# Optimization experiments

Measured on AMD Instinct MI355X. Metric: run time of the kernel, lower is better.

Reference implementation:

```python
import jax, jax.numpy as jnp
import numpy as np

C = 16            # cell state dim
ALPHA_T = 0.1     # alive threshold
_SOBEL = jnp.array([[-1., 0., 1.], [-2., 0., 2.], [-1., 0., 1.]], jnp.float32) / 8.0


def _depthwise(x, k2d):
    # x: [B,H,W,C], k2d: [3,3] same filter per channel (groups=C depthwise conv)
    k = jnp.tile(k2d[:, :, None, None], (1, 1, 1, C)).astype(x.dtype)  # [3,3,1,C] HWIO
    return jax.lax.conv_general_dilated(
        x, k, window_strides=(1, 1), padding='SAME',
        feature_group_count=C, dimension_numbers=('NHWC', 'HWIO', 'NHWC'))


def _alive_mask(state):
    # 3x3 max-pool on alpha channel (index 3), stride 1, SAME padding
    alpha = state[..., 3:4]
    pooled = jax.lax.reduce_window(alpha, -jnp.inf, jax.lax.max,
                                   (1, 3, 3, 1), (1, 1, 1, 1), 'SAME')
    return (pooled >= ALPHA_T).astype(state.dtype)


def setup_inputs() -> dict:
    key = jax.random.key(0)
    k1, k2, k3, k4, k5 = jax.random.split(key, 5)
    B, H, W, S = 128, 40, 40, 32
    initial_state = jax.random.uniform(k1, (B, H, W, C), jnp.float32)
    # MLP params (torch Linear layout: [out, in]); scaled to keep 32-step rollout finite
    W1 = jax.random.normal(k2, (128, 3 * C), jnp.float32) * 0.1
    b1 = jax.random.normal(k3, (128,), jnp.float32) * 0.1
    W2 = jax.random.normal(k4, (C, 128), jnp.float32) * 0.02
    # Bernoulli(0.5) stochastic update mask == (rand > update_probability=0.5)
    upd_mask = jax.random.randint(k5, (S, B, H, W), 0, 2, jnp.int32)
    return {"initial_state": initial_state, "W1": W1, "b1": b1, "W2": W2,
            "upd_mask": upd_mask, "steps": S, "batch_size": B}


def reference(initial_state, W1, b1, W2, upd_mask, steps, batch_size):
    def step(state, mask_t):
        am = _alive_mask(state)
        masked = state * am
        sx = _depthwise(masked, _SOBEL)
        sy = _depthwise(masked, _SOBEL.T)
        perception = jnp.concatenate([masked, sx, sy], axis=-1)       # [B,H,W,48]
        hid = jax.nn.relu(jnp.einsum('bhwi,oi->bhwo', perception, W1) + b1)
        update = jnp.einsum('bhwi,oi->bhwo', hid, W2)                 # [B,H,W,16]
        update = update * mask_t[..., None].astype(state.dtype)
        new_state = state + update
        new_state = new_state * _alive_mask(new_state)
        return new_state, new_state

    _, ys = jax.lax.scan(step, initial_state, upd_mask)
    stacked = jnp.concatenate([initial_state[None], ys], axis=0)      # [steps+1,B,H,W,16]
    alpha = jnp.clip(stacked[..., 3:4], 0.0, 1.0)
    rgb = (jnp.clip(1.0 - alpha + stacked[..., :3], 0.0, 1.0) * 255.0).astype(jnp.uint8)
    return rgb, stacked
```

## Files before the change

kernel.cpp:

```cpp
#include <hip/hip_runtime.h>

#define Cn 16
#define Bn 128
#define Hn 40
#define Wn 40
#define Sn 32
#define HID 128
#define PIX (Bn * Hn * Wn)
#define NFRAME (Sn + 1)
#define RGB_TOTAL (NFRAME * PIX * 3)
#define STACK_FRAME (PIX * Cn)
#define ALPHA_T 0.1f

__global__ __launch_bounds__(256) void step_update(
    const float* __restrict__ S,
    const float* __restrict__ amF,
    const int*   __restrict__ maskT,
    float*       __restrict__ P,
    float*       __restrict__ Pa,
    const float* __restrict__ W1,
    const float* __restrict__ b1,
    const float* __restrict__ W2T)
{
    int idx = blockIdx.x * 256 + threadIdx.x;
    int x  = idx % Wn;
    int t1 = idx / Wn;
    int y  = t1 % Hn;

    float am[3][3];
#pragma unroll
    for (int dy = 0; dy < 3; ++dy) {
#pragma unroll
        for (int dx = 0; dx < 3; ++dx) {
            int yy = y + dy - 1, xx = x + dx - 1;
            bool in = (yy >= 0) && (yy < Hn) && (xx >= 0) && (xx < Wn);
            am[dy][dx] = in ? amF[idx + (dy - 1) * Wn + (dx - 1)] : 0.f;
        }
    }

    float perc[48];
    float4 cen[4];
#pragma unroll
    for (int cg = 0; cg < 4; ++cg) {
        float4 m[3][3];
#pragma unroll
        for (int dy = 0; dy < 3; ++dy) {
#pragma unroll
            for (int dx = 0; dx < 3; ++dx) {
                int yy = y + dy - 1, xx = x + dx - 1;
                bool in = (yy >= 0) && (yy < Hn) && (xx >= 0) && (xx < Wn);
                float4 v;
                if (in) {
                    v = *(const float4*)&S[(idx + (dy - 1) * Wn + (dx - 1)) * Cn + cg * 4];
                    if (dy == 1 && dx == 1) cen[cg] = v;
                    float a = am[dy][dx];
                    v.x *= a; v.y *= a; v.z *= a; v.w *= a;
                } else {
                    v.x = 0.f; v.y = 0.f; v.z = 0.f; v.w = 0.f;
                }
                m[dy][dx] = v;
            }
        }
        perc[cg * 4 + 0] = m[1][1].x;
        perc[cg * 4 + 1] = m[1][1].y;
        perc[cg * 4 + 2] = m[1][1].z;
        perc[cg * 4 + 3] = m[1][1].w;
        perc[16 + cg * 4 + 0] = ((m[0][2].x - m[0][0].x) + 2.f * (m[1][2].x - m[1][0].x) + (m[2][2].x - m[2][0].x)) * 0.125f;
        perc[16 + cg * 4 + 1] = ((m[0][2].y - m[0][0].y) + 2.f * (m[1][2].y - m[1][0].y) + (m[2][2].y - m[2][0].y)) * 0.125f;
        perc[16 + cg * 4 + 2] = ((m[0][2].z - m[0][0].z) + 2.f * (m[1][2].z - m[1][0].z) + (m[2][2].z - m[2][0].z)) * 0.125f;
        perc[16 + cg * 4 + 3] = ((m[0][2].w - m[0][0].w) + 2.f * (m[1][2].w - m[1][0].w) + (m[2][2].w - m[2][0].w)) * 0.125f;
        perc[32 + cg * 4 + 0] = ((m[2][0].x - m[0][0].x) + 2.f * (m[2][1].x - m[0][1].x) + (m[2][2].x - m[0][2].x)) * 0.125f;
        perc[32 + cg * 4 + 1] = ((m[2][0].y - m[0][0].y) + 2.f * (m[2][1].y - m[0][1].y) + (m[2][2].y - m[0][2].y)) * 0.125f;
        perc[32 + cg * 4 + 2] = ((m[2][0].z - m[0][0].z) + 2.f * (m[2][1].z - m[0][1].z) + (m[2][2].z - m[0][2].z)) * 0.125f;
        perc[32 + cg * 4 + 3] = ((m[2][0].w - m[0][0].w) + 2.f * (m[2][1].w - m[0][1].w) + (m[2][2].w - m[0][2].w)) * 0.125f;
    }

    float upd[16];
#pragma unroll
    for (int c = 0; c < 16; ++c) upd[c] = 0.f;

    for (int j = 0; j < HID; ++j) {
        const float* w = &W1[j * 48];
        float hh0 = b1[j], hh1 = 0.f, hh2 = 0.f, hh3 = 0.f;
#pragma unroll
        for (int i = 0; i < 12; ++i) {
            hh0 = fmaf(perc[i],      w[i],      hh0);
            hh1 = fmaf(perc[12 + i], w[12 + i], hh1);
            hh2 = fmaf(perc[24 + i], w[24 + i], hh2);
            hh3 = fmaf(perc[36 + i], w[36 + i], hh3);
        }
        float h = fmaxf((hh0 + hh1) + (hh2 + hh3), 0.f);

        const float* w2 = &W2T[j * 16];
#pragma unroll
        for (int c = 0; c < 16; ++c) upd[c] = fmaf(h, w2[c], upd[c]);
    }

    float fm = (float)maskT[idx];

#pragma unroll
    for (int cg = 0; cg < 4; ++cg) {
        float4 s = cen[cg];
        float4 o;
        o.x = s.x + upd[cg * 4 + 0] * fm;
        o.y = s.y + upd[cg * 4 + 1] * fm;
        o.z = s.z + upd[cg * 4 + 2] * fm;
        o.w = s.w + upd[cg * 4 + 3] * fm;
        *(float4*)&P[idx * Cn + cg * 4] = o;
        if (cg == 0) Pa[idx] = o.w;
    }
}

__global__ __launch_bounds__(256) void step_mask(
    const float* __restrict__ P,
    const float* __restrict__ Pa,
    float*       __restrict__ Snext,
    float*       __restrict__ amNext)
{
    int idx = blockIdx.x * 256 + threadIdx.x;
    int x  = idx % Wn;
    int t1 = idx / Wn;
    int y  = t1 % Hn;

    float a[5][5];
#pragma unroll
    for (int dy = 0; dy < 5; ++dy) {
#pragma unroll
        for (int dx = 0; dx < 5; ++dx) {
            int yy = y + dy - 2, xx = x + dx - 2;
            bool in = (yy >= 0) && (yy < Hn) && (xx >= 0) && (xx < Wn);
            a[dy][dx] = in ? Pa[idx + (dy - 2) * Wn + (dx - 2)] : -1e30f;
        }
    }

    float s[3][3];
    float aliveC = 0.f;
#pragma unroll
    for (int qy = 0; qy < 3; ++qy) {
#pragma unroll
        for (int qx = 0; qx < 3; ++qx) {
            float p = a[qy][qx];
            p = fmaxf(p, a[qy][qx + 1]);
            p = fmaxf(p, a[qy][qx + 2]);
            p = fmaxf(p, a[qy + 1][qx]);
            p = fmaxf(p, a[qy + 1][qx + 1]);
            p = fmaxf(p, a[qy + 1][qx + 2]);
            p = fmaxf(p, a[qy + 2][qx]);
            p = fmaxf(p, a[qy + 2][qx + 1]);
            p = fmaxf(p, a[qy + 2][qx + 2]);
            float alive = (p >= ALPHA_T) ? 1.f : 0.f;
            if (qy == 1 && qx == 1) aliveC = alive;
            int yy = y + qy - 1, xx = x + qx - 1;
            bool in = (yy >= 0) && (yy < Hn) && (xx >= 0) && (xx < Wn);
            s[qy][qx] = in ? a[qy + 1][qx + 1] * alive : -1e30f;
        }
    }

    float ps = s[0][0];
    ps = fmaxf(ps, s[0][1]); ps = fmaxf(ps, s[0][2]);
    ps = fmaxf(ps, s[1][0]); ps = fmaxf(ps, s[1][1]); ps = fmaxf(ps, s[1][2]);
    ps = fmaxf(ps, s[2][0]); ps = fmaxf(ps, s[2][1]); ps = fmaxf(ps, s[2][2]);
    float amN = (ps >= ALPHA_T) ? 1.f : 0.f;

#pragma unroll
    for (int cg = 0; cg < 4; ++cg) {
        float4 v = *(const float4*)&P[idx * Cn + cg * 4];
        v.x *= aliveC; v.y *= aliveC; v.z *= aliveC; v.w *= aliveC;
        *(float4*)&Snext[idx * Cn + cg * 4] = v;
    }
    amNext[idx] = amN;
}

__global__ __launch_bounds__(256) void init_am(
    const float* __restrict__ S0, float* __restrict__ amF)
{
    int idx = blockIdx.x * 256 + threadIdx.x;
    int x  = idx % Wn;
    int t1 = idx / Wn;
    int y  = t1 % Hn;
    float pooled = -1e30f;
#pragma unroll
    for (int dy = -1; dy <= 1; ++dy) {
#pragma unroll
        for (int dx = -1; dx <= 1; ++dx) {
            int yy = y + dy, xx = x + dx;
            bool in = (yy >= 0) && (yy < Hn) && (xx >= 0) && (xx < Wn);
            if (in) pooled = fmaxf(pooled, S0[(idx + dy * Wn + dx) * Cn + 3]);
        }
    }
    amF[idx] = (pooled >= ALPHA_T) ? 1.f : 0.f;
}

__global__ __launch_bounds__(256) void transpose_w2(
    const float* __restrict__ W2, float* __restrict__ W2T)
{
    int i = blockIdx.x * 256 + threadIdx.x;
    if (i < Cn * HID) {
        int c = i >> 7;
        int j = i & 127;
        W2T[j * Cn + c] = W2[i];
    }
}

__global__ __launch_bounds__(256) void copy_init(
    const float4* __restrict__ src, float4* __restrict__ dst, int n4)
{
    int i = blockIdx.x * 256 + threadIdx.x;
    if (i < n4) dst[i] = src[i];
}

__global__ __launch_bounds__(256) void rgb_kernel(
    const float* __restrict__ stacked, float* __restrict__ rgb, int npix)
{
    int idx = blockIdx.x * 256 + threadIdx.x;
    if (idx >= npix) return;
    float4 s = *(const float4*)&stacked[idx * Cn];
    float a = fminf(fmaxf(s.w, 0.f), 1.f);
    float base = 1.f - a;
    rgb[idx * 3 + 0] = truncf(fminf(fmaxf(base + s.x, 0.f), 1.f) * 255.f);
    rgb[idx * 3 + 1] = truncf(fminf(fmaxf(base + s.y, 0.f), 1.f) * 255.f);
    rgb[idx * 3 + 2] = truncf(fminf(fmaxf(base + s.z, 0.f), 1.f) * 255.f);
}

extern "C" void kernel_launch(void* const* d_in, const int* in_sizes, int n_in,
                              void* d_out, int out_size, void* d_ws, size_t ws_size,
                              hipStream_t stream) {
    const float* init = (const float*)d_in[0];
    const float* W1   = (const float*)d_in[1];
    const float* b1   = (const float*)d_in[2];
    const float* W2   = (const float*)d_in[3];
    const int*   upd  = (const int*)d_in[4];

    float* out     = (float*)d_out;
    float* rgb     = out;
    float* stacked = out + RGB_TOTAL;
    float* P   = out;
    float* Pa  = out + (size_t)PIX * Cn;
    float* amF = out + (size_t)PIX * (Cn + 1);
    float* W2T = out + (size_t)PIX * (Cn + 2);

    const int blocks_pix = PIX / 256;

    copy_init<<<(PIX * Cn / 4 + 255) / 256, 256, 0, stream>>>(
        (const float4*)init, (float4*)stacked, PIX * Cn / 4);
    init_am<<<blocks_pix, 256, 0, stream>>>(stacked, amF);
    transpose_w2<<<(Cn * HID + 255) / 256, 256, 0, stream>>>(W2, W2T);

    for (int t = 0; t < Sn; ++t) {
        step_update<<<blocks_pix, 256, 0, stream>>>(
            stacked + (size_t)t * STACK_FRAME, amF, upd + (size_t)t * PIX,
            P, Pa, W1, b1, W2T);
        step_mask<<<blocks_pix, 256, 0, stream>>>(
            P, Pa, stacked + (size_t)(t + 1) * STACK_FRAME, amF);
    }

    const int npix_all = NFRAME * PIX;
    rgb_kernel<<<(npix_all + 255) / 256, 256, 0, stream>>>(stacked, rgb, npix_all);
}
```

Baseline: 4.015 ms.

## Compact active-update pixels and split hidden layer across two threads per pixel

Precomputes, for every step, a compacted list of pixels whose stochastic update mask is set, using a ballot count, a per-step scan and a fill pass. The MLP kernel then runs only on those pixels, roughly half of them. Each pixel's 128 hidden units are split between two threads, and the partial updates are reduced through shared memory. Inactive pixels take their state from the previous frame inside the mask kernel, and an alpha plane is double-buffered so unchanged pixels keep correct alpha. The cost is extra preprocessing kernels, workspace for the lists, and a full-grid launch where trailing blocks exit idle.

New measurement: 5.446 ms. +35.6%, slower.

```diff
diff --git a/kernel.cpp b/kernel.cpp
--- a/kernel.cpp
+++ b/kernel.cpp
@@ -11,117 +11,202 @@
 #define RGB_TOTAL (NFRAME * PIX * 3)
 #define STACK_FRAME (PIX * Cn)
 #define ALPHA_T 0.1f
-
-__global__ __launch_bounds__(256) void step_update(
+#define NCHUNK (PIX / 256)
+
+
+__global__ __launch_bounds__(256) void mask_count(
+    const int* __restrict__ upd, int* __restrict__ counts)
+{
+    int i = blockIdx.x * 256 + threadIdx.x;
+    bool m = upd[i] != 0;
+    unsigned long long b = __ballot(m);
+    __shared__ int wc[4];
+    int lane = threadIdx.x & 63, w = threadIdx.x >> 6;
+    if (lane == 0) wc[w] = __popcll(b);
+    __syncthreads();
+    if (threadIdx.x == 0) counts[blockIdx.x] = wc[0] + wc[1] + wc[2] + wc[3];
+}
+
+__global__ __launch_bounds__(1024) void scan_counts(
+    const int* __restrict__ counts, int* __restrict__ base, int* __restrict__ nAct)
+{
+    int t = blockIdx.x;
+    __shared__ int bufA[NCHUNK];
+    __shared__ int bufB[NCHUNK];
+    for (int c = threadIdx.x; c < NCHUNK; c += 1024) bufA[c] = counts[t * NCHUNK + c];
+    __syncthreads();
+    int* src = bufA; int* dst = bufB;
+    for (int off = 1; off < NCHUNK; off <<= 1) {
+        for (int c = threadIdx.x; c < NCHUNK; c += 1024)
+            dst[c] = src[c] + ((c >= off) ? src[c - off] : 0);
+        __syncthreads();
+        int* tmp = src; src = dst; dst = tmp;
+    }
+    for (int c = threadIdx.x; c < NCHUNK; c += 1024)
+        base[t * NCHUNK + c] = (c == 0) ? 0 : src[c - 1];
+    if (threadIdx.x == 0) nAct[t] = src[NCHUNK - 1];
+}
+
+__global__ __launch_bounds__(256) void mask_fill(
+    const int* __restrict__ upd, const int* __restrict__ base, int* __restrict__ list)
+{
+    int blk = blockIdx.x;
+    int t   = blk / NCHUNK;
+    int i   = blk * 256 + threadIdx.x;
+    int pix = i - t * PIX;
+    bool m = upd[i] != 0;
+    unsigned long long b = __ballot(m);
+    int lane = threadIdx.x & 63, w = threadIdx.x >> 6;
+    int rank = __popcll(b & (((unsigned long long)1 << lane) - 1ull));
+    __shared__ int wcnt[4], wexc[4];
+    if (lane == 0) wcnt[w] = __popcll(b);
+    __syncthreads();
+    if (threadIdx.x == 0) {
+        int s = 0;
+        for (int k = 0; k < 4; ++k) { wexc[k] = s; s += wcnt[k]; }
+    }
+    __syncthreads();
+    if (m) list[t * PIX + base[blk] + wexc[w] + rank] = pix;
+}
+
+__global__ __launch_bounds__(256) void step_update_c(
     const float* __restrict__ S,
     const float* __restrict__ amF,
-    const int*   __restrict__ maskT,
+    const int*   __restrict__ nActP,
+    const int*   __restrict__ list,
     float*       __restrict__ P,
-    float*       __restrict__ Pa,
+    float*       __restrict__ PaM,
     const float* __restrict__ W1,
     const float* __restrict__ b1,
     const float* __restrict__ W2T)
+{
+    __shared__ float redUpd[128][16];
+
+    int nAct  = *nActP;
+    int p     = threadIdx.x & 127;
+    int halfI = threadIdx.x >> 7;
+    int i     = blockIdx.x * 128 + p;
+    bool act  = i < nAct;
+
+    int idx = 0;
+    float upd[16];
+    float4 cen[4];
+
+    if (act) {
+        idx = list[i];
+        int x  = idx % Wn;
+        int t1 = idx / Wn;
+        int y  = t1 % Hn;
+
+        float am[3][3];
+#pragma unroll
+        for (int dy = 0; dy < 3; ++dy) {
+#pragma unroll
+            for (int dx = 0; dx < 3; ++dx) {
+                int yy = y + dy - 1, xx = x + dx - 1;
+                bool in = (yy >= 0) && (yy < Hn) && (xx >= 0) && (xx < Wn);
+                am[dy][dx] = in ? amF[idx + (dy - 1) * Wn + (dx - 1)] : 0.f;
+            }
+        }
+
+        float perc[48];
+#pragma unroll
+        for (int cg = 0; cg < 4; ++cg) {
+            float4 m[3][3];
+#pragma unroll
+            for (int dy = 0; dy < 3; ++dy) {
+#pragma unroll
+                for (int dx = 0; dx < 3; ++dx) {
+                    int yy = y + dy - 1, xx = x + dx - 1;
+                    bool in = (yy >= 0) && (yy < Hn) && (xx >= 0) && (xx < Wn);
+                    float4 v;
+                    if (in) {
+                        v = *(const float4*)&S[(idx + (dy - 1) * Wn + (dx - 1)) * Cn + cg * 4];
+                        if (dy == 1 && dx == 1) cen[cg] = v;
+                        float a = am[dy][dx];
+                        v.x *= a; v.y *= a; v.z *= a; v.w *= a;
+                    } else {
+                        v.x = 0.f; v.y = 0.f; v.z = 0.f; v.w = 0.f;
+                    }
+                    m[dy][dx] = v;
+                }
+            }
+            perc[cg * 4 + 0] = m[1][1].x;
+            perc[cg * 4 + 1] = m[1][1].y;
+            perc[cg * 4 + 2] = m[1][1].z;
+            perc[cg * 4 + 3] = m[1][1].w;
+            perc[16 + cg * 4 + 0] = ((m[0][2].x - m[0][0].x) + 2.f * (m[1][2].x - m[1][0].x) + (m[2][2].x - m[2][0].x)) * 0.125f;
+            perc[16 + cg * 4 + 1] = ((m[0][2].y - m[0][0].y) + 2.f * (m[1][2].y - m[1][0].y) + (m[2][2].y - m[2][0].y)) * 0.125f;
+            perc[16 + cg * 4 + 2] = ((m[0][2].z - m[0][0].z) + 2.f * (m[1][2].z - m[1][0].z) + (m[2][2].z - m[2][0].z)) * 0.125f;
+            perc[16 + cg * 4 + 3] = ((m[0][2].w - m[0][0].w) + 2.f * (m[1][2].w - m[1][0].w) + (m[2][2].w - m[2][0].w)) * 0.125f;
+            perc[32 + cg * 4 + 0] = ((m[2][0].x - m[0][0].x) + 2.f * (m[2][1].x - m[0][1].x) + (m[2][2].x - m[0][2].x)) * 0.125f;
+            perc[32 + cg * 4 + 1] = ((m[2][0].y - m[0][0].y) + 2.f * (m[2][1].y - m[0][1].y) + (m[2][2].y - m[0][2].y)) * 0.125f;
+            perc[32 + cg * 4 + 2] = ((m[2][0].z - m[0][0].z) + 2.f * (m[2][1].z - m[0][1].z) + (m[2][2].z - m[0][2].z)) * 0.125f;
+            perc[32 + cg * 4 + 3] = ((m[2][0].w - m[0][0].w) + 2.f * (m[2][1].w - m[0][1].w) + (m[2][2].w - m[0][2].w)) * 0.125f;
+        }
+
+#pragma unroll
+        for (int c = 0; c < 16; ++c) upd[c] = 0.f;
+
+        const float* W1h = W1  + halfI * (64 * 48);
+        const float* b1h = b1  + halfI * 64;
+        const float* W2h = W2T + halfI * (64 * 16);
+
+#pragma unroll 2
+        for (int j = 0; j < 64; ++j) {
+            const float* w = &W1h[j * 48];
+            float hh0 = b1h[j], hh1 = 0.f, hh2 = 0.f, hh3 = 0.f;
+#pragma unroll
+            for (int q = 0; q < 12; ++q) {
+                hh0 = fmaf(perc[q],      w[q],      hh0);
+                hh1 = fmaf(perc[12 + q], w[12 + q], hh1);
+                hh2 = fmaf(perc[24 + q], w[24 + q], hh2);
+                hh3 = fmaf(perc[36 + q], w[36 + q], hh3);
+            }
+            float h = fmaxf((hh0 + hh1) + (hh2 + hh3), 0.f);
+            const float* w2 = &W2h[j * 16];
+#pragma unroll
+            for (int c = 0; c < 16; ++c) upd[c] = fmaf(h, w2[c], upd[c]);
+        }
+
+        if (halfI == 1) {
+#pragma unroll
+            for (int cg = 0; cg < 4; ++cg)
+                *(float4*)&redUpd[p][cg * 4] = *(float4*)&upd[cg * 4];
+        }
+    }
+
+    __syncthreads();
+
+    if (act && halfI == 0) {
+#pragma unroll
+        for (int cg = 0; cg < 4; ++cg) {
+            float4 o = *(float4*)&redUpd[p][cg * 4];
+            float4 s = cen[cg];
+            o.x = s.x + (upd[cg * 4 + 0] + o.x);
+            o.y = s.y + (upd[cg * 4 + 1] + o.y);
+            o.z = s.z + (upd[cg * 4 + 2] + o.z);
+            o.w = s.w + (upd[cg * 4 + 3] + o.w);
+            *(float4*)&P[idx * Cn + cg * 4] = o;
+            if (cg == 0) PaM[idx] = o.w;
+        }
+    }
+}
+
+__global__ __launch_bounds__(256) void step_mask(
+    const float* __restrict__ P,
+    const float* __restrict__ PaCur,
+    const float* __restrict__ S,
+    const int*   __restrict__ maskT,
+    float*       __restrict__ Snext,
+    float*       __restrict__ amNext,
+    float*       __restrict__ PaNxt)
 {
     int idx = blockIdx.x * 256 + threadIdx.x;
     int x  = idx % Wn;
     int t1 = idx / Wn;
     int y  = t1 % Hn;
 
-    float am[3][3];
-#pragma unroll
-    for (int dy = 0; dy < 3; ++dy) {
-#pragma unroll
-        for (int dx = 0; dx < 3; ++dx) {
-            int yy = y + dy - 1, xx = x + dx - 1;
-            bool in = (yy >= 0) && (yy < Hn) && (xx >= 0) && (xx < Wn);
-            am[dy][dx] = in ? amF[idx + (dy - 1) * Wn + (dx - 1)] : 0.f;
-        }
-    }
-
-    float perc[48];
-    float4 cen[4];
-#pragma unroll
-    for (int cg = 0; cg < 4; ++cg) {
-        float4 m[3][3];
-#pragma unroll
-        for (int dy = 0; dy < 3; ++dy) {
-#pragma unroll
-            for (int dx = 0; dx < 3; ++dx) {
-                int yy = y + dy - 1, xx = x + dx - 1;
-                bool in = (yy >= 0) && (yy < Hn) && (xx >= 0) && (xx < Wn);
-                float4 v;
-                if (in) {
-                    v = *(const float4*)&S[(idx + (dy - 1) * Wn + (dx - 1)) * Cn + cg * 4];
-                    if (dy == 1 && dx == 1) cen[cg] = v;
-                    float a = am[dy][dx];
-                    v.x *= a; v.y *= a; v.z *= a; v.w *= a;
-                } else {
-                    v.x = 0.f; v.y = 0.f; v.z = 0.f; v.w = 0.f;
-                }
-                m[dy][dx] = v;
-            }
-        }
-        perc[cg * 4 + 0] = m[1][1].x;
-        perc[cg * 4 + 1] = m[1][1].y;
-        perc[cg * 4 + 2] = m[1][1].z;
-        perc[cg * 4 + 3] = m[1][1].w;
-        perc[16 + cg * 4 + 0] = ((m[0][2].x - m[0][0].x) + 2.f * (m[1][2].x - m[1][0].x) + (m[2][2].x - m[2][0].x)) * 0.125f;
-        perc[16 + cg * 4 + 1] = ((m[0][2].y - m[0][0].y) + 2.f * (m[1][2].y - m[1][0].y) + (m[2][2].y - m[2][0].y)) * 0.125f;
-        perc[16 + cg * 4 + 2] = ((m[0][2].z - m[0][0].z) + 2.f * (m[1][2].z - m[1][0].z) + (m[2][2].z - m[2][0].z)) * 0.125f;
-        perc[16 + cg * 4 + 3] = ((m[0][2].w - m[0][0].w) + 2.f * (m[1][2].w - m[1][0].w) + (m[2][2].w - m[2][0].w)) * 0.125f;
-        perc[32 + cg * 4 + 0] = ((m[2][0].x - m[0][0].x) + 2.f * (m[2][1].x - m[0][1].x) + (m[2][2].x - m[0][2].x)) * 0.125f;
-        perc[32 + cg * 4 + 1] = ((m[2][0].y - m[0][0].y) + 2.f * (m[2][1].y - m[0][1].y) + (m[2][2].y - m[0][2].y)) * 0.125f;
-        perc[32 + cg * 4 + 2] = ((m[2][0].z - m[0][0].z) + 2.f * (m[2][1].z - m[0][1].z) + (m[2][2].z - m[0][2].z)) * 0.125f;
-        perc[32 + cg * 4 + 3] = ((m[2][0].w - m[0][0].w) + 2.f * (m[2][1].w - m[0][1].w) + (m[2][2].w - m[0][2].w)) * 0.125f;
-    }
-
-    float upd[16];
-#pragma unroll
-    for (int c = 0; c < 16; ++c) upd[c] = 0.f;
-
-    for (int j = 0; j < HID; ++j) {
-        const float* w = &W1[j * 48];
-        float hh0 = b1[j], hh1 = 0.f, hh2 = 0.f, hh3 = 0.f;
-#pragma unroll
-        for (int i = 0; i < 12; ++i) {
-            hh0 = fmaf(perc[i],      w[i],      hh0);
-            hh1 = fmaf(perc[12 + i], w[12 + i], hh1);
-            hh2 = fmaf(perc[24 + i], w[24 + i], hh2);
-            hh3 = fmaf(perc[36 + i], w[36 + i], hh3);
-        }
-        float h = fmaxf((hh0 + hh1) + (hh2 + hh3), 0.f);
-
-        const float* w2 = &W2T[j * 16];
-#pragma unroll
-        for (int c = 0; c < 16; ++c) upd[c] = fmaf(h, w2[c], upd[c]);
-    }
-
-    float fm = (float)maskT[idx];
-
-#pragma unroll
-    for (int cg = 0; cg < 4; ++cg) {
-        float4 s = cen[cg];
-        float4 o;
-        o.x = s.x + upd[cg * 4 + 0] * fm;
-        o.y = s.y + upd[cg * 4 + 1] * fm;
-        o.z = s.z + upd[cg * 4 + 2] * fm;
-        o.w = s.w + upd[cg * 4 + 3] * fm;
-        *(float4*)&P[idx * Cn + cg * 4] = o;
-        if (cg == 0) Pa[idx] = o.w;
-    }
-}
-
-__global__ __launch_bounds__(256) void step_mask(
-    const float* __restrict__ P,
-    const float* __restrict__ Pa,
-    float*       __restrict__ Snext,
-    float*       __restrict__ amNext)
-{
-    int idx = blockIdx.x * 256 + threadIdx.x;
-    int x  = idx % Wn;
-    int t1 = idx / Wn;
-    int y  = t1 % Hn;
-
     float a[5][5];
 #pragma unroll
     for (int dy = 0; dy < 5; ++dy) {
@@ -129,7 +214,7 @@
         for (int dx = 0; dx < 5; ++dx) {
             int yy = y + dy - 2, xx = x + dx - 2;
             bool in = (yy >= 0) && (yy < Hn) && (xx >= 0) && (xx < Wn);
-            a[dy][dx] = in ? Pa[idx + (dy - 2) * Wn + (dx - 2)] : -1e30f;
+            a[dy][dx] = in ? PaCur[idx + (dy - 2) * Wn + (dx - 2)] : -1e30f;
         }
     }
 
@@ -139,16 +224,16 @@
     for (int qy = 0; qy < 3; ++qy) {
 #pragma unroll
         for (int qx = 0; qx < 3; ++qx) {
-            float p = a[qy][qx];
-            p = fmaxf(p, a[qy][qx + 1]);
-            p = fmaxf(p, a[qy][qx + 2]);
-            p = fmaxf(p, a[qy + 1][qx]);
-            p = fmaxf(p, a[qy + 1][qx + 1]);
-            p = fmaxf(p, a[qy + 1][qx + 2]);
-            p = fmaxf(p, a[qy + 2][qx]);
-            p = fmaxf(p, a[qy + 2][qx + 1]);
-            p = fmaxf(p, a[qy + 2][qx + 2]);
-            float alive = (p >= ALPHA_T) ? 1.f : 0.f;
+            float pm = a[qy][qx];
+            pm = fmaxf(pm, a[qy][qx + 1]);
+            pm = fmaxf(pm, a[qy][qx + 2]);
+            pm = fmaxf(pm, a[qy + 1][qx]);
+            pm = fmaxf(pm, a[qy + 1][qx + 1]);
+            pm = fmaxf(pm, a[qy + 1][qx + 2]);
+            pm = fmaxf(pm, a[qy + 2][qx]);
+            pm = fmaxf(pm, a[qy + 2][qx + 1]);
+            pm = fmaxf(pm, a[qy + 2][qx + 2]);
+            float alive = (pm >= ALPHA_T) ? 1.f : 0.f;
             if (qy == 1 && qx == 1) aliveC = alive;
             int yy = y + qy - 1, xx = x + qx - 1;
             bool in = (yy >= 0) && (yy < Hn) && (xx >= 0) && (xx < Wn);
@@ -162,17 +247,24 @@
     ps = fmaxf(ps, s[2][0]); ps = fmaxf(ps, s[2][1]); ps = fmaxf(ps, s[2][2]);
     float amN = (ps >= ALPHA_T) ? 1.f : 0.f;
 
+    bool fm = maskT[idx] != 0;
 #pragma unroll
     for (int cg = 0; cg < 4; ++cg) {
-        float4 v = *(const float4*)&P[idx * Cn + cg * 4];
-        v.x *= aliveC; v.y *= aliveC; v.z *= aliveC; v.w *= aliveC;
+        float4 pv = *(const float4*)&P[idx * Cn + cg * 4];
+        float4 sv = *(const float4*)&S[idx * Cn + cg * 4];
+        float4 v;
+        v.x = (fm ? pv.x : sv.x) * aliveC;
+        v.y = (fm ? pv.y : sv.y) * aliveC;
+        v.z = (fm ? pv.z : sv.z) * aliveC;
+        v.w = (fm ? pv.w : sv.w) * aliveC;
         *(float4*)&Snext[idx * Cn + cg * 4] = v;
+        if (cg == 0) PaNxt[idx] = v.w;
     }
     amNext[idx] = amN;
 }
 
-__global__ __launch_bounds__(256) void init_am(
-    const float* __restrict__ S0, float* __restrict__ amF)
+__global__ __launch_bounds__(256) void init_plane(
+    const float* __restrict__ S0, float* __restrict__ amF, float* __restrict__ Pa0)
 {
     int idx = blockIdx.x * 256 + threadIdx.x;
     int x  = idx % Wn;
@@ -189,6 +281,7 @@
         }
     }
     amF[idx] = (pooled >= ALPHA_T) ? 1.f : 0.f;
+    Pa0[idx] = S0[idx * Cn + 3];
 }
 
 __global__ __launch_bounds__(256) void transpose_w2(
@@ -234,24 +327,37 @@
     float* out     = (float*)d_out;
     float* rgb     = out;
     float* stacked = out + RGB_TOTAL;
-    float* P   = out;
-    float* Pa  = out + (size_t)PIX * Cn;
-    float* amF = out + (size_t)PIX * (Cn + 1);
-    float* W2T = out + (size_t)PIX * (Cn + 2);
+    float* P    = out;
+    float* Pa0  = out + (size_t)PIX * Cn;
+    float* Pa1  = Pa0 + PIX;
+    float* amF  = Pa1 + PIX;
+    float* W2T  = amF + PIX;
+    int*   list   = (int*)(W2T + 2048);
+    int*   counts = list + (size_t)Sn * PIX;
+    int*   base   = counts + Sn * NCHUNK;
+    int*   nAct   = base + Sn * NCHUNK;
 
     const int blocks_pix = PIX / 256;
 
     copy_init<<<(PIX * Cn / 4 + 255) / 256, 256, 0, stream>>>(
         (const float4*)init, (float4*)stacked, PIX * Cn / 4);
-    init_am<<<blocks_pix, 256, 0, stream>>>(stacked, amF);
+    init_plane<<<blocks_pix, 256, 0, stream>>>(stacked, amF, Pa0);
     transpose_w2<<<(Cn * HID + 255) / 256, 256, 0, stream>>>(W2, W2T);
 
+    mask_count<<<Sn * NCHUNK, 256, 0, stream>>>(upd, counts);
+    scan_counts<<<Sn, 1024, 0, stream>>>(counts, base, nAct);
+    mask_fill<<<Sn * NCHUNK, 256, 0, stream>>>(upd, base, list);
+
+    float* PaCur = Pa0;
+    float* PaNxt = Pa1;
     for (int t = 0; t < Sn; ++t) {
-        step_update<<<blocks_pix, 256, 0, stream>>>(
-            stacked + (size_t)t * STACK_FRAME, amF, upd + (size_t)t * PIX,
-            P, Pa, W1, b1, W2T);
+        step_update_c<<<PIX / 128, 256, 0, stream>>>(
+            stacked + (size_t)t * STACK_FRAME, amF, nAct + t, list + (size_t)t * PIX,
+            P, PaCur, W1, b1, W2T);
         step_mask<<<blocks_pix, 256, 0, stream>>>(
-            P, Pa, stacked + (size_t)(t + 1) * STACK_FRAME, amF);
+            P, PaCur, stacked + (size_t)t * STACK_FRAME, upd + (size_t)t * PIX,
+            stacked + (size_t)(t + 1) * STACK_FRAME, amF, PaNxt);
+        float* tmp = PaCur; PaCur = PaNxt; PaNxt = tmp;
     }
 
     const int npix_all = NFRAME * PIX;
```
